# Performance work log

Hardware: AMD Instinct MI355X
Metric: run time of the kernel (lower is better)

## Reference

```python
import jax, jax.numpy as jnp
import numpy as np

EPS = 1e-4
CIN = [3, 192, 160, 96, 192, 192, 192, 192, 192]
COUT = [192, 160, 96, 192, 192, 192, 192, 192, 10]
K = [5, 1, 1, 5, 1, 1, 3, 1, 1]
PAD = [2, 0, 0, 2, 0, 0, 1, 0, 0]
NAMES = ["x"] + [f"{p}{i}" for i in range(1, 10) for p in ("g", "be", "m", "v", "w", "b")] + ["ma", "va", "mb", "vb"]


def _bn(x, m, v, g=None, b=None):
    # inference-mode BatchNorm2d, eps=1e-4
    inv = jax.lax.rsqrt(v + EPS)[None, :, None, None]
    y = (x - m[None, :, None, None]) * inv
    if g is not None:
        y = y * g[None, :, None, None] + b[None, :, None, None]
    return y


def _binactive(x):
    # XNOR-Net BinActive: sign of activations
    return jnp.sign(x)


def _conv(x, w, b, pad):
    y = jax.lax.conv_general_dilated(x, w, (1, 1), [(pad, pad), (pad, pad)], dimension_numbers=("NCHW", "OIHW", "NCHW"))
    return y + b[None, :, None, None]


def _maxpool(x):
    # MaxPool2d(kernel_size=3, stride=2, padding=1)
    return jax.lax.reduce_window(x, -jnp.inf, jax.lax.max, (1, 1, 3, 3), (1, 1, 2, 2), [(0, 0), (0, 0), (1, 1), (1, 1)])


def _avgpool(x):
    # AvgPool2d(3, stride=2, padding=1), count_include_pad=True -> divide by 9
    s = jax.lax.reduce_window(x, 0.0, jax.lax.add, (1, 1, 3, 3), (1, 1, 2, 2), [(0, 0), (0, 0), (1, 1), (1, 1)])
    return s / 9.0


def _forward(P):
    def bc(i, x):
        # BinConv2d: BN(affine) -> BinActive -> (dropout=identity in eval) -> Conv -> ReLU
        x = _bn(x, P[f"m{i}"], P[f"v{i}"], P[f"g{i}"], P[f"be{i}"])
        x = _binactive(x)
        x = _conv(x, P[f"w{i}"], P[f"b{i}"], PAD[i - 1])
        return jax.nn.relu(x)

    x = bc(1, P["x"])  # [B,192,32,32]
    x = jax.nn.relu(_bn(x, P["ma"], P["va"]))  # BN affine=False + ReLU
    x = bc(3, bc(2, x))
    x = _maxpool(x)  # 32 -> 16
    x = bc(6, bc(5, bc(4, x)))
    x = _avgpool(x)  # 16 -> 8
    x = bc(8, bc(7, x))
    x = _bn(x, P["mb"], P["vb"])  # BN affine=False
    x = bc(9, x)  # [B,10,8,8]  (trailing extra ReLU is a no-op after bc's ReLU)
    return jnp.mean(x, axis=(2, 3))  # AvgPool2d(8) + view -> [B,10]


def setup_inputs() -> dict:
    key = jax.random.key(0)
    ks = iter(jax.random.split(key, 64))
    inp = {"x": jax.random.normal(next(ks), (256, 3, 32, 32), jnp.float32)}
    for i in range(9):
        c_in, c_out, k = CIN[i], COUT[i], K[i]
        inp[f"g{i+1}"] = jax.random.normal(next(ks), (c_in,), jnp.float32)
        inp[f"be{i+1}"] = jax.random.normal(next(ks), (c_in,), jnp.float32)
        inp[f"m{i+1}"] = jax.random.normal(next(ks), (c_in,), jnp.float32)
        inp[f"v{i+1}"] = jax.random.uniform(next(ks), (c_in,), jnp.float32)
        inp[f"w{i+1}"] = jax.random.normal(next(ks), (c_out, c_in, k, k), jnp.float32) * 0.05
        inp[f"b{i+1}"] = jax.random.normal(next(ks), (c_out,), jnp.float32) * 0.05
    inp["ma"] = jax.random.normal(next(ks), (192,), jnp.float32)
    inp["va"] = jax.random.uniform(next(ks), (192,), jnp.float32)
    inp["mb"] = jax.random.normal(next(ks), (192,), jnp.float32)
    inp["vb"] = jax.random.uniform(next(ks), (192,), jnp.float32)
    return inp


def reference(x, g1, be1, m1, v1, w1, b1, g2, be2, m2, v2, w2, b2, g3, be3, m3, v3, w3, b3, g4, be4, m4, v4, w4, b4, g5, be5, m5, v5, w5, b5, g6, be6, m6, v6, w6, b6, g7, be7, m7, v7, w7, b7, g8, be8, m8, v8, w8, b8, g9, be9, m9, v9, w9, b9, ma, va, mb, vb):
    return _forward(dict(locals()))
```

## Files before the change

### kernel.cpp

```cpp
#include <hip/hip_runtime.h>
#include <stdint.h>

typedef _Float16 f16;
typedef _Float16 f16x4 __attribute__((ext_vector_type(4)));
typedef _Float16 f16x8 __attribute__((ext_vector_type(8)));
typedef float f32x4 __attribute__((ext_vector_type(4)));

__device__ __forceinline__ float fsgn(float t) {
  return (t > 0.f) ? 1.f : ((t < 0.f) ? -1.f : 0.f);
}

__device__ __forceinline__ void ldsld16(const void* g, void* l) {
  __builtin_amdgcn_global_load_lds(
      (const __attribute__((address_space(1))) unsigned int*)(unsigned long long)(uintptr_t)g,
      (__attribute__((address_space(3))) unsigned int*)(unsigned int)(uintptr_t)l,
      16, 0, 0);
}

struct PP {
  const float* g[9];
  const float* be[9];
  const float* m[9];
  const float* v[9];
  const float* b[9];
  const float* ma;
  const float* va;
  const float* mb;
  const float* vb;
};

struct PrepAll {
  const float* w[9];
  f16* wh[9];
  f16* wl[9];
  const float* x;
  f16* s1p;
  PP pp;
  float* prm;
};

__device__ void prep_params_body(const PP& a, float* prm) {
  const int c = threadIdx.x;
  if (c >= 192) return;
  const int CINv[9]  = {3, 192, 160, 96, 192, 192, 192, 192, 192};
  const int COUTv[9] = {192, 160, 96, 192, 192, 192, 192, 192, 10};
  auto alpha = [&](int i) { return a.g[i][c] / sqrtf(a.v[i][c] + 1e-4f); };
  auto beta  = [&](int i, float A) { return a.be[i][c] - a.m[i][c] * A; };

  for (int i = 0; i < 9; ++i) {
    float* base = prm + i * 5 * 192;
    base[c] = (c < COUTv[i]) ? a.b[i][c] : 0.f;
    float P1 = 0.f, P2 = 0.f, P3 = 0.f, P4 = 0.f;
    int bn = -1;
    if (i == 0) bn = 1;
    else if (i == 1) bn = 2;
    else if (i == 3) bn = 4;
    else if (i == 4) bn = 5;
    else if (i == 6) bn = 7;
    if (bn >= 0 && c < CINv[bn]) { float A = alpha(bn); P1 = A; P2 = beta(bn, A); }
    if (i == 7) {
      float ib = 1.f / sqrtf(a.vb[c] + 1e-4f);
      float A9 = alpha(8);
      P1 = ib * A9;
      P2 = a.be[8][c] - A9 * (a.m[8][c] + a.mb[c] * ib);
    }
    if (i == 0) {
      P3 = 1.f / sqrtf(a.va[c] + 1e-4f);
      P4 = a.ma[c] * P3;
    }
    base[192 + c] = P1;
    base[384 + c] = P2;
    base[576 + c] = P3;
    base[768 + c] = P4;
  }
  { float A = (c < 96) ? alpha(3) : 0.f;
    prm[45 * 192 + c] = A; prm[46 * 192 + c] = (c < 96) ? beta(3, A) : 0.f; }
  { float A = alpha(6);
    prm[47 * 192 + c] = A; prm[48 * 192 + c] = beta(6, A); }
  { float A = (c < 3) ? alpha(0) : 0.f;
    prm[49 * 192 + c] = A; prm[50 * 192 + c] = (c < 3) ? beta(0, A) : 0.f; }
}

__device__ void prep_w_body(const float* __restrict__ w, f16* __restrict__ wh,
                            f16* __restrict__ wl, int idx,
                            int Co, int Cin, int KH, int KW, int KP, int mode) {
  const int co = idx / KP;
  const int k = idx - co * KP;
  float val = 0.f;
  if (co < Co) {
    if (mode == 0) {
      if (k < Cin) val = w[(size_t)co * Cin + k];
    } else if (mode == 1) {
      int tap = k / Cin, cc = k - tap * Cin;
      int kh = tap / KW, kw = tap - kh * KW;
      val = w[(((size_t)co * Cin + cc) * KH + kh) * KW + kw];
    } else {
      int kh = k >> 4, r = k & 15;
      if (kh < 5 && r < 15) {
        int kw = r / 3, cc = r - kw * 3;
        val = w[(((size_t)co * 3 + cc) * 5 + kh) * 5 + kw];
      }
    }
  }
  f16 h = (f16)val;
  float hf = (float)h;
  if (fabsf(hf) < 6.1035e-5f) { h = (f16)0.f; hf = 0.f; }
  f16 l = (f16)((val - hf) * 4096.f);
  wh[idx] = h;
  wl[idx] = l;
}

__constant__ int WB[10] = {1, 73, 217, 297, 2097, 2241, 2385, 3681, 3825, 3873};

__global__ void prep_all(PrepAll A) {
  const int b = blockIdx.x;
  if (b == 0) { prep_params_body(A.pp, A.prm); return; }
  if (b < 3873) {
    static const int COv[9]  = {192, 192, 128, 192, 192, 192, 192, 192, 64};
    static const int Cov[9]  = {192, 160, 96, 192, 192, 192, 192, 192, 10};
    static const int CIv[9]  = {3, 192, 160, 96, 192, 192, 192, 192, 192};
    static const int KHv[9]  = {5, 1, 1, 5, 1, 1, 3, 1, 1};
    static const int KPv[9]  = {96, 192, 160, 2400, 192, 192, 1728, 192, 192};
    static const int MDv[9]  = {2, 0, 0, 1, 0, 0, 1, 0, 0};
    int i = 0;
    while (b >= WB[i + 1]) ++i;
    const int idx = (b - WB[i]) * 256 + threadIdx.x;
    if (idx < COv[i] * KPv[i])
      prep_w_body(A.w[i], A.wh[i], A.wl[i], idx, Cov[i], CIv[i], KHv[i], KHv[i], KPv[i], MDv[i]);
    return;
  }
  const int idx = (b - 3873) * 256 + threadIdx.x;
  if (idx >= 256 * 36 * 36 * 3) return;
  int c = idx % 3;
  int t = idx / 3;
  int wp = t % 36; t /= 36;
  int hp = t % 36;
  int n = t / 36;
  int h = hp - 2, w = wp - 2;
  f16 s = (f16)0.f;
  if (h >= 0 && h < 32 && w >= 0 && w < 32) {
    float al = A.pp.g[0][c] / sqrtf(A.pp.v[0][c] + 1e-4f);
    float be = A.pp.be[0][c] - A.pp.m[0][c] * al;
    float xv = A.x[((size_t)(n * 3 + c) * 32 + h) * 32 + w];
    s = (f16)fsgn(xv * al + be);
  }
  A.s1p[idx] = s;
}

template <int HIN, int CH, int HOUT, int HPAD, int POFF, bool AVG>
__global__ void poolk(const float* __restrict__ in, f16* __restrict__ out,
                      const float* __restrict__ pa, const float* __restrict__ pb) {
  constexpr int C4 = CH / 4;
  const int idx = blockIdx.x * 256 + threadIdx.x;
  if (idx >= 256 * HPAD * HPAD * C4) return;
  int c4 = idx % C4;
  int t = idx / C4;
  int wp = t % HPAD; t /= HPAD;
  int hp = t % HPAD;
  int n = t / HPAD;
  int h = hp - POFF, w = wp - POFF;
  f16x4 res;
  res[0] = res[1] = res[2] = res[3] = (f16)0.f;
  if (h >= 0 && h < HOUT && w >= 0 && w < HOUT) {
    float acc[4];
#pragma unroll
    for (int i = 0; i < 4; ++i) acc[i] = AVG ? 0.f : -1e30f;
#pragma unroll
    for (int i = 0; i < 3; ++i) {
      int yh = 2 * h - 1 + i;
      if (yh < 0 || yh >= HIN) continue;
#pragma unroll
      for (int j = 0; j < 3; ++j) {
        int yw = 2 * w - 1 + j;
        if (yw < 0 || yw >= HIN) continue;
        f32x4 vv = *(const f32x4*)(in + ((size_t)(n * HIN + yh) * HIN + yw) * CH + c4 * 4);
#pragma unroll
        for (int k = 0; k < 4; ++k) acc[k] = AVG ? (acc[k] + vv[k]) : fmaxf(acc[k], vv[k]);
      }
    }
    f32x4 A = *(const f32x4*)(pa + c4 * 4);
    f32x4 B = *(const f32x4*)(pb + c4 * 4);
#pragma unroll
    for (int k = 0; k < 4; ++k) {
      float xv = AVG ? (acc[k] / 9.f) : acc[k];
      res[k] = (f16)fsgn(xv * A[k] + B[k]);
    }
  }
  *(f16x4*)(out + (size_t)idx * 4) = res;
}

template <int MODE, int EPI, int LOG_HW, int LOG_W, int CIN, int COP, int COUT,
          int KH, int KW, int HP, int WP, int NCH, int CCH>
__global__ __launch_bounds__(256, 2) void convk(
    const f16* __restrict__ sin, const f16* __restrict__ wh, const f16* __restrict__ wl,
    const float* __restrict__ prm, void* __restrict__ outp) {
  static_assert(NCH >= 3, "pipeline needs >=3 chunks");
  constexpr int NCOB = COP / 64;
  constexpr int HWm = (1 << LOG_HW) - 1;
  constexpr int Wm = (1 << LOG_W) - 1;

  const int tid = threadIdx.x;
  const int wid = tid >> 6;
  const int lane = tid & 63;
  const int bid = (blockIdx.x & 7) * ((int)gridDim.x >> 3) + (blockIdx.x >> 3);
  const int mb = bid / NCOB;
  const int cob = bid - mb * NCOB;

  __shared__ __align__(16) char smem[73728];

  const int pr = lane >> 2;
  const int pg = lane & 3;

  const f16* psrc[4];
#pragma unroll
  for (int q = 0; q < 4; ++q) {
    const int j = wid * 4 + q;
    const int r = j * 16 + pr;
    const int g = pg ^ ((r >> 1) & 3);
    const int m = mb * 256 + r;
    if constexpr (MODE == 0) {
      psrc[q] = sin + (size_t)m * CIN + g * 8;
    } else if constexpr (MODE == 1) {
      const int n = m >> LOG_HW;
      const int hw = m & HWm;
      const int h = hw >> LOG_W;
      const int w = hw & Wm;
      psrc[q] = sin + ((size_t)(n * HP + h) * WP + w) * CIN + g * 8;
    } else {
      const int n = m >> 10;
      const int hw = m & 1023;
      const int h = hw >> 5;
      const int w = hw & 31;
      const int khg = g >> 1;
      const int sel = g & 1;
      psrc[q] = sin + ((size_t)(n * 36 + h + khg) * 36 + (w + (sel ? 2 : 0))) * 3 + (sel ? 2 : 0);
    }
  }
  const int wr = wid * 16 + pr;
  const int wgg = pg ^ ((wr >> 1) & 3);
  const f16* wsrc_h = wh + (size_t)(cob * 64 + wr) * (NCH * 32) + wgg * 8;
  const f16* wsrc_l = wl + (size_t)(cob * 64 + wr) * (NCH * 32) + wgg * 8;

  auto stage = [&](int kc, int cur) {
    char* lb = smem + cur * 24576;
    int coff;
    if constexpr (MODE == 0) coff = kc * 32;
    else if constexpr (MODE == 2) coff = kc * 216;
    else {
      const int tap = kc / CCH;
      const int cc = kc - tap * CCH;
      const int kh = tap / KW;
      const int kw = tap - kh * KW;
      coff = (kh * WP + kw) * CIN + cc * 32;
    }
#pragma unroll
    for (int q = 0; q < 4; ++q) ldsld16(psrc[q] + coff, lb + (wid * 4 + q) * 1024);
    ldsld16(wsrc_h + kc * 32, lb + 16384 + wid * 1024);
    ldsld16(wsrc_l + kc * 32, lb + 20480 + wid * 1024);
  };

  const int ln15 = lane & 15;
  const int xg = (lane >> 4) ^ ((ln15 >> 1) & 3);
  const int rdB = wid * 4096 + ln15 * 64 + xg * 16;
  const int rdA = 16384 + ln15 * 64 + xg * 16;

  f32x4 aH[4][4], aL[4][4];
#pragma unroll
  for (int a = 0; a < 4; ++a)
#pragma unroll
    for (int b = 0; b < 4; ++b) {
      aH[a][b] = (f32x4){0.f, 0.f, 0.f, 0.f};
      aL[a][b] = (f32x4){0.f, 0.f, 0.f, 0.f};
    }

  auto compute = [&](int cur) {
    const char* cb = smem + cur * 24576;
    f16x8 Bf[4];
#pragma unroll
    for (int a = 0; a < 4; ++a) Bf[a] = *(const f16x8*)(cb + a * 1024 + rdB);
    __builtin_amdgcn_s_setprio(1);
#pragma unroll
    for (int b = 0; b < 4; ++b) {
      const f16x8 Ah = *(const f16x8*)(cb + rdA + b * 1024);
      const f16x8 Al = *(const f16x8*)(cb + rdA + 4096 + b * 1024);
#pragma unroll
      for (int a = 0; a < 4; ++a) {
        aH[a][b] = __builtin_amdgcn_mfma_f32_16x16x32_f16(Ah, Bf[a], aH[a][b], 0, 0, 0);
        aL[a][b] = __builtin_amdgcn_mfma_f32_16x16x32_f16(Al, Bf[a], aL[a][b], 0, 0, 0);
      }
    }
    __builtin_amdgcn_s_setprio(0);
  };

  stage(0, 0);
  stage(1, 1);

  for (int s = 0; s < NCH; ++s) {
    if (s == NCH - 1) asm volatile("s_waitcnt vmcnt(0)" ::: "memory");
    else              asm volatile("s_waitcnt vmcnt(6)" ::: "memory");
    __builtin_amdgcn_s_barrier();
    if (s + 2 < NCH) stage(s + 2, (s + 2) % 3);
    compute(s % 3);
  }

  constexpr float LSC = 1.f / 4096.f;
  const int hi4 = (lane >> 4) * 4;

  if constexpr (EPI == 3) {
    float red[4] = {0.f, 0.f, 0.f, 0.f};
    const f32x4 bi = *(const f32x4*)(prm + hi4);
#pragma unroll
    for (int a = 0; a < 4; ++a)
#pragma unroll
      for (int i = 0; i < 4; ++i)
        red[i] += fmaxf(aH[a][0][i] + aL[a][0][i] * LSC + bi[i], 0.f);
#pragma unroll
    for (int i = 0; i < 4; ++i) {
      red[i] += __shfl_xor(red[i], 1);
      red[i] += __shfl_xor(red[i], 2);
      red[i] += __shfl_xor(red[i], 4);
      red[i] += __shfl_xor(red[i], 8);
    }
    if (ln15 == 0) {
      const int n = mb * 4 + wid;
      float* o = (float*)outp;
#pragma unroll
      for (int i = 0; i < 4; ++i) {
        const int co = hi4 + i;
        if (co < 10) o[n * 10 + co] = red[i] * (1.f / 64.f);
      }
    }
  } else {
#pragma unroll
    for (int a = 0; a < 4; ++a) {
      const int m = mb * 256 + wid * 64 + a * 16 + ln15;
#pragma unroll
      for (int b = 0; b < 4; ++b) {
        const int co = cob * 64 + b * 16 + hi4;
        if (co < COUT) {
          const f32x4 bi = *(const f32x4*)(prm + co);
          f32x4 v;
#pragma unroll
          for (int i = 0; i < 4; ++i)
            v[i] = fmaxf(aH[a][b][i] + aL[a][b][i] * LSC + bi[i], 0.f);
          if constexpr (EPI == 1) {
            const f32x4 ia = *(const f32x4*)(prm + 576 + co);
            const f32x4 mi = *(const f32x4*)(prm + 768 + co);
#pragma unroll
            for (int i = 0; i < 4; ++i) v[i] = fmaxf(v[i] * ia[i] - mi[i], 0.f);
          }
          if constexpr (EPI == 2) {
            *(f32x4*)((float*)outp + (size_t)m * COUT + co) = v;
          } else {
            const f32x4 al = *(const f32x4*)(prm + 192 + co);
            const f32x4 be = *(const f32x4*)(prm + 384 + co);
            f16x4 sgn;
#pragma unroll
            for (int i = 0; i < 4; ++i) sgn[i] = (f16)fsgn(v[i] * al[i] + be[i]);
            *(f16x4*)((f16*)outp + (size_t)m * COUT + co) = sgn;
          }
        }
      }
    }
  }
}

extern "C" void kernel_launch(void* const* d_in, const int* in_sizes, int n_in,
                              void* d_out, int out_size, void* d_ws, size_t ws_size,
                              hipStream_t stream) {
  (void)in_sizes; (void)n_in; (void)out_size; (void)ws_size;
  auto IN = [&](int i) { return (const float*)d_in[i]; };
  char* ws = (char*)d_ws;

  const size_t OFF_W = 65536;
  static const size_t WSZ[9] = {36864, 73728, 40960, 921600, 73728, 73728, 663552, 73728, 24576};
  f16* WH[9]; f16* WL[9];
  {
    size_t o = OFF_W;
    for (int i = 0; i < 9; ++i) { WH[i] = (f16*)(ws + o); WL[i] = (f16*)(ws + o + WSZ[i]); o += 2 * WSZ[i]; }
  }
  const size_t OFF_ACT = OFF_W + 3964928;
  const size_t SLOT_A = OFF_ACT;
  const size_t SLOT_B = SLOT_A + 83890176;

  f16*   S1P = (f16*)(ws + SLOT_A);
  f16*   S2  = (f16*)(ws + SLOT_B);
  f16*   S3  = (f16*)(ws + SLOT_A);
  float* Y3  = (float*)(ws + SLOT_B);
  f16*   S4P = (f16*)(ws + SLOT_A);
  f16*   S5  = (f16*)(ws + SLOT_B);
  f16*   S6  = (f16*)(ws + SLOT_A);
  float* Y6  = (float*)(ws + SLOT_B);
  f16*   S7P = (f16*)(ws + SLOT_A);
  f16*   S8  = (f16*)(ws + SLOT_B);
  f16*   S9  = (f16*)(ws + SLOT_A);

  float* PRM = (float*)ws;

  PrepAll PA;
  for (int i = 0; i < 9; ++i) {
    PA.pp.g[i]  = IN(1 + i * 6 + 0);
    PA.pp.be[i] = IN(1 + i * 6 + 1);
    PA.pp.m[i]  = IN(1 + i * 6 + 2);
    PA.pp.v[i]  = IN(1 + i * 6 + 3);
    PA.pp.b[i]  = IN(1 + i * 6 + 5);
    PA.w[i] = IN(1 + i * 6 + 4);
    PA.wh[i] = WH[i];
    PA.wl[i] = WL[i];
  }
  PA.pp.ma = IN(55); PA.pp.va = IN(56); PA.pp.mb = IN(57); PA.pp.vb = IN(58);
  PA.x = IN(0);
  PA.s1p = S1P;
  PA.prm = PRM;

  prep_all<<<7761, 256, 0, stream>>>(PA);

  convk<2, 1, 10, 5, 3, 192, 192, 5, 5, 36, 36, 3, 1><<<1024 * 3, 256, 0, stream>>>(
      S1P, WH[0], WL[0], PRM + 0 * 960, S2);
  convk<0, 0, 10, 5, 192, 192, 160, 1, 1, 0, 0, 6, 1><<<1024 * 3, 256, 0, stream>>>(
      S2, WH[1], WL[1], PRM + 1 * 960, S3);
  convk<0, 2, 10, 5, 160, 128, 96, 1, 1, 0, 0, 5, 1><<<1024 * 2, 256, 0, stream>>>(
      S3, WH[2], WL[2], PRM + 2 * 960, Y3);
  poolk<32, 96, 16, 20, 2, false><<<9600, 256, 0, stream>>>(Y3, S4P, PRM + 45 * 192, PRM + 46 * 192);
  convk<1, 0, 8, 4, 96, 192, 192, 5, 5, 20, 20, 75, 3><<<256 * 3, 256, 0, stream>>>(
      S4P, WH[3], WL[3], PRM + 3 * 960, S5);
  convk<0, 0, 8, 4, 192, 192, 192, 1, 1, 0, 0, 6, 1><<<256 * 3, 256, 0, stream>>>(
      S5, WH[4], WL[4], PRM + 4 * 960, S6);
  convk<0, 2, 8, 4, 192, 192, 192, 1, 1, 0, 0, 6, 1><<<256 * 3, 256, 0, stream>>>(
      S6, WH[5], WL[5], PRM + 5 * 960, Y6);
  poolk<16, 192, 8, 10, 1, true><<<4800, 256, 0, stream>>>(Y6, S7P, PRM + 47 * 192, PRM + 48 * 192);
  convk<1, 0, 6, 3, 192, 192, 192, 3, 3, 10, 10, 54, 6><<<64 * 3, 256, 0, stream>>>(
      S7P, WH[6], WL[6], PRM + 6 * 960, S8);
  convk<0, 0, 6, 3, 192, 192, 192, 1, 1, 0, 0, 6, 1><<<64 * 3, 256, 0, stream>>>(
      S8, WH[7], WL[7], PRM + 7 * 960, S9);
  convk<0, 3, 6, 3, 192, 64, 10, 1, 1, 0, 0, 6, 1><<<64, 256, 0, stream>>>(
      S9, WH[8], WL[8], PRM + 8 * 960, d_out);
}
```

Baseline: 601.7 us.

## Merge hi/lo weight accumulators and double-buffer LDS fragment reads in registers

```diff
diff --git a/kernel.cpp b/kernel.cpp
--- a/kernel.cpp
+++ b/kernel.cpp
@@ -105,7 +105,7 @@
   f16 h = (f16)val;
   float hf = (float)h;
   if (fabsf(hf) < 6.1035e-5f) { h = (f16)0.f; hf = 0.f; }
-  f16 l = (f16)((val - hf) * 4096.f);
+  f16 l = (f16)(val - hf);
   wh[idx] = h;
   wl[idx] = l;
 }
@@ -264,46 +264,58 @@
   const int rdB = wid * 4096 + ln15 * 64 + xg * 16;
   const int rdA = 16384 + ln15 * 64 + xg * 16;
 
-  f32x4 aH[4][4], aL[4][4];
+  f32x4 acc[4][4];
 #pragma unroll
   for (int a = 0; a < 4; ++a)
 #pragma unroll
+    for (int b = 0; b < 4; ++b) acc[a][b] = (f32x4){0.f, 0.f, 0.f, 0.f};
+
+  f16x8 rEv[12], rOd[12];
+
+  auto readRegs = [&](int cur, f16x8 (&R)[12]) {
+    const char* cb = smem + cur * 24576;
+#pragma unroll
+    for (int a = 0; a < 4; ++a) R[a] = *(const f16x8*)(cb + a * 1024 + rdB);
+#pragma unroll
     for (int b = 0; b < 4; ++b) {
-      aH[a][b] = (f32x4){0.f, 0.f, 0.f, 0.f};
-      aL[a][b] = (f32x4){0.f, 0.f, 0.f, 0.f};
-    }
-
-  auto compute = [&](int cur) {
-    const char* cb = smem + cur * 24576;
-    f16x8 Bf[4];
-#pragma unroll
-    for (int a = 0; a < 4; ++a) Bf[a] = *(const f16x8*)(cb + a * 1024 + rdB);
+      R[4 + 2 * b] = *(const f16x8*)(cb + rdA + b * 1024);
+      R[5 + 2 * b] = *(const f16x8*)(cb + rdA + 4096 + b * 1024);
+    }
+  };
+
+  auto mfmaBlk = [&](const f16x8 (&R)[12]) {
     __builtin_amdgcn_s_setprio(1);
 #pragma unroll
-    for (int b = 0; b < 4; ++b) {
-      const f16x8 Ah = *(const f16x8*)(cb + rdA + b * 1024);
-      const f16x8 Al = *(const f16x8*)(cb + rdA + 4096 + b * 1024);
-#pragma unroll
-      for (int a = 0; a < 4; ++a) {
-        aH[a][b] = __builtin_amdgcn_mfma_f32_16x16x32_f16(Ah, Bf[a], aH[a][b], 0, 0, 0);
-        aL[a][b] = __builtin_amdgcn_mfma_f32_16x16x32_f16(Al, Bf[a], aL[a][b], 0, 0, 0);
-      }
-    }
+    for (int b = 0; b < 4; ++b)
+#pragma unroll
+      for (int a = 0; a < 4; ++a)
+        acc[a][b] = __builtin_amdgcn_mfma_f32_16x16x32_f16(R[4 + 2 * b], R[a], acc[a][b], 0, 0, 0);
+#pragma unroll
+    for (int b = 0; b < 4; ++b)
+#pragma unroll
+      for (int a = 0; a < 4; ++a)
+        acc[a][b] = __builtin_amdgcn_mfma_f32_16x16x32_f16(R[5 + 2 * b], R[a], acc[a][b], 0, 0, 0);
     __builtin_amdgcn_s_setprio(0);
   };
 
   stage(0, 0);
   stage(1, 1);
-
-  for (int s = 0; s < NCH; ++s) {
+  asm volatile("s_waitcnt vmcnt(6)" ::: "memory");
+  __builtin_amdgcn_s_barrier();
+  readRegs(0, rEv);
+  stage(2, 2);
+
+  for (int s = 1; s < NCH; ++s) {
     if (s == NCH - 1) asm volatile("s_waitcnt vmcnt(0)" ::: "memory");
     else              asm volatile("s_waitcnt vmcnt(6)" ::: "memory");
     __builtin_amdgcn_s_barrier();
+    if (s & 1) { readRegs(s % 3, rOd); mfmaBlk(rEv); }
+    else       { readRegs(s % 3, rEv); mfmaBlk(rOd); }
     if (s + 2 < NCH) stage(s + 2, (s + 2) % 3);
-    compute(s % 3);
-  }
-
-  constexpr float LSC = 1.f / 4096.f;
+  }
+  if ((NCH - 1) & 1) mfmaBlk(rOd);
+  else               mfmaBlk(rEv);
+
   const int hi4 = (lane >> 4) * 4;
 
   if constexpr (EPI == 3) {
@@ -313,7 +325,7 @@
     for (int a = 0; a < 4; ++a)
 #pragma unroll
       for (int i = 0; i < 4; ++i)
-        red[i] += fmaxf(aH[a][0][i] + aL[a][0][i] * LSC + bi[i], 0.f);
+        red[i] += fmaxf(acc[a][0][i] + bi[i], 0.f);
 #pragma unroll
     for (int i = 0; i < 4; ++i) {
       red[i] += __shfl_xor(red[i], 1);
@@ -342,7 +354,7 @@
           f32x4 v;
 #pragma unroll
           for (int i = 0; i < 4; ++i)
-            v[i] = fmaxf(aH[a][b][i] + aL[a][b][i] * LSC + bi[i], 0.f);
+            v[i] = fmaxf(acc[a][b][i] + bi[i], 0.f);
           if constexpr (EPI == 1) {
             const f32x4 ia = *(const f32x4*)(prm + 576 + co);
             const f32x4 mi = *(const f32x4*)(prm + 768 + co);
```

Result: slower. 1.483 ms (+146.5%).

## Interleave global-to-LDS prefetch with MFMA phases inside the K-loop

Applied to the files above, without the earlier changes.

```diff
diff --git a/kernel.cpp b/kernel.cpp
--- a/kernel.cpp
+++ b/kernel.cpp
@@ -241,18 +241,21 @@
   const f16* wsrc_h = wh + (size_t)(cob * 64 + wr) * (NCH * 32) + wgg * 8;
   const f16* wsrc_l = wl + (size_t)(cob * 64 + wr) * (NCH * 32) + wgg * 8;
 
-  auto stage = [&](int kc, int cur) {
-    char* lb = smem + cur * 24576;
-    int coff;
-    if constexpr (MODE == 0) coff = kc * 32;
-    else if constexpr (MODE == 2) coff = kc * 216;
+  auto coffOf = [&](int kc) -> int {
+    if constexpr (MODE == 0) return kc * 32;
+    else if constexpr (MODE == 2) return kc * 216;
     else {
       const int tap = kc / CCH;
       const int cc = kc - tap * CCH;
       const int kh = tap / KW;
       const int kw = tap - kh * KW;
-      coff = (kh * WP + kw) * CIN + cc * 32;
-    }
+      return (kh * WP + kw) * CIN + cc * 32;
+    }
+  };
+
+  auto stage = [&](int kc, int cur) {
+    char* lb = smem + cur * 24576;
+    const int coff = coffOf(kc);
 #pragma unroll
     for (int q = 0; q < 4; ++q) ldsld16(psrc[q] + coff, lb + (wid * 4 + q) * 1024);
     ldsld16(wsrc_h + kc * 32, lb + 16384 + wid * 1024);
@@ -273,25 +276,6 @@
       aL[a][b] = (f32x4){0.f, 0.f, 0.f, 0.f};
     }
 
-  auto compute = [&](int cur) {
-    const char* cb = smem + cur * 24576;
-    f16x8 Bf[4];
-#pragma unroll
-    for (int a = 0; a < 4; ++a) Bf[a] = *(const f16x8*)(cb + a * 1024 + rdB);
-    __builtin_amdgcn_s_setprio(1);
-#pragma unroll
-    for (int b = 0; b < 4; ++b) {
-      const f16x8 Ah = *(const f16x8*)(cb + rdA + b * 1024);
-      const f16x8 Al = *(const f16x8*)(cb + rdA + 4096 + b * 1024);
-#pragma unroll
-      for (int a = 0; a < 4; ++a) {
-        aH[a][b] = __builtin_amdgcn_mfma_f32_16x16x32_f16(Ah, Bf[a], aH[a][b], 0, 0, 0);
-        aL[a][b] = __builtin_amdgcn_mfma_f32_16x16x32_f16(Al, Bf[a], aL[a][b], 0, 0, 0);
-      }
-    }
-    __builtin_amdgcn_s_setprio(0);
-  };
-
   stage(0, 0);
   stage(1, 1);
 
@@ -299,8 +283,43 @@
     if (s == NCH - 1) asm volatile("s_waitcnt vmcnt(0)" ::: "memory");
     else              asm volatile("s_waitcnt vmcnt(6)" ::: "memory");
     __builtin_amdgcn_s_barrier();
-    if (s + 2 < NCH) stage(s + 2, (s + 2) % 3);
-    compute(s % 3);
+    const char* cb = smem + (s % 3) * 24576;
+    const bool doStage = (s + 2 < NCH);
+    char* nlb = smem + ((s + 2) % 3) * 24576;
+    const int coff2 = doStage ? coffOf(s + 2) : 0;
+
+    f16x8 Bf[4];
+#pragma unroll
+    for (int a = 0; a < 4; ++a) Bf[a] = *(const f16x8*)(cb + a * 1024 + rdB);
+
+#pragma unroll
+    for (int p = 0; p < 4; ++p) {
+      const f16x8 Ah = *(const f16x8*)(cb + rdA + p * 1024);
+      const f16x8 Al = *(const f16x8*)(cb + rdA + 4096 + p * 1024);
+      if (doStage) {
+        if (p == 0) {
+          ldsld16(psrc[0] + coff2, nlb + (wid * 4 + 0) * 1024);
+          ldsld16(psrc[1] + coff2, nlb + (wid * 4 + 1) * 1024);
+        } else if (p == 1) {
+          ldsld16(psrc[2] + coff2, nlb + (wid * 4 + 2) * 1024);
+          ldsld16(psrc[3] + coff2, nlb + (wid * 4 + 3) * 1024);
+        } else if (p == 2) {
+          ldsld16(wsrc_h + (s + 2) * 32, nlb + 16384 + wid * 1024);
+          ldsld16(wsrc_l + (s + 2) * 32, nlb + 20480 + wid * 1024);
+        }
+      }
+      __builtin_amdgcn_s_barrier();
+      __builtin_amdgcn_s_setprio(1);
+#pragma unroll
+      for (int a = 0; a < 4; ++a)
+        aH[a][p] = __builtin_amdgcn_mfma_f32_16x16x32_f16(Ah, Bf[a], aH[a][p], 0, 0, 0);
+#pragma unroll
+      for (int a = 0; a < 4; ++a)
+        aL[a][p] = __builtin_amdgcn_mfma_f32_16x16x32_f16(Al, Bf[a], aL[a][p], 0, 0, 0);
+      __builtin_amdgcn_s_setprio(0);
+      __builtin_amdgcn_sched_barrier(0);
+      if (p < 3) __builtin_amdgcn_s_barrier();
+    }
   }
 
   constexpr float LSC = 1.f / 4096.f;
```

Measured after the change: 607.1 us. Within noise of the previous version (+0.9%).
